# Kernel tuning notes

Measured on AMD Instinct MI355X. Metric: run time of the kernel, lower is better.

The kernel has to match this reference:

```python
import jax, jax.numpy as jnp
import numpy as np

B, T, D_MODEL, N_HEAD = 8, 1024, 1024, 8
D_K = D_MODEL // N_HEAD  # = d_v = 128; V projection shared across heads


def setup_inputs() -> dict:
    key = jax.random.key(0)
    ks = jax.random.split(key, 8)
    scale = 0.02
    q = jax.random.normal(ks[0], (B, T, D_MODEL), jnp.float32)
    k = jax.random.normal(ks[1], (B, T, D_MODEL), jnp.float32)
    v = jax.random.normal(ks[2], (B, T, D_MODEL), jnp.float32)
    # causal mask, 1.0 = attend, broadcast to batch (shape (B, T, T))
    mask = jnp.broadcast_to(jnp.tril(jnp.ones((T, T), jnp.float32)), (B, T, T))
    Wq = jax.random.normal(ks[3], (N_HEAD, D_MODEL, D_K), jnp.float32) * scale
    Wk = jax.random.normal(ks[4], (N_HEAD, D_MODEL, D_K), jnp.float32) * scale
    Wv = jax.random.normal(ks[5], (D_MODEL, D_K), jnp.float32) * scale  # shared across heads
    Wo = jax.random.normal(ks[6], (D_K, D_MODEL), jnp.float32) * scale
    return {"q": q, "k": k, "v": v, "mask": mask, "Wq": Wq, "Wk": Wk, "Wv": Wv, "Wo": Wo}


def reference(q, k, v, mask, Wq, Wk, Wv, Wo):
    # Per-head Q/K projections (batched over heads), shared V projection.
    qh = jnp.einsum('btd,hdk->hbtk', q, Wq)  # (H,B,T,d_k)
    kh = jnp.einsum('bsd,hdk->hbsk', k, Wk)  # (H,B,S,d_k)
    vh = jnp.einsum('bsd,dk->bsk', v, Wv)    # (B,S,d_v) shared across heads
    temper = jnp.sqrt(jnp.asarray(qh.shape[-1], jnp.float32))
    scores = jnp.einsum('hbtk,hbsk->hbts', qh, kh) / temper
    scores = scores + (-1e9) * (1.0 - mask)[None]  # additive mask per head
    attn = jax.nn.softmax(scores, axis=-1)          # (H,B,T,S)
    heads = jnp.einsum('hbts,bsk->hbtk', attn, vh)  # (H,B,T,d_v)
    out = jnp.einsum('btk,kd->btd', heads.mean(axis=0), Wo)  # mean over heads, then w_o
    return out, attn  # dropout rate 0.0 / inference -> identity
```

## Files before the change

### kernel.cpp

```cpp
#include <hip/hip_runtime.h>
#include <cstdint>

typedef __attribute__((ext_vector_type(8))) short bf16x8;
typedef __attribute__((ext_vector_type(4))) float f32x4;

constexpr int NH = 8, NB = 8, SEQ = 1024, DM = 1024, DK = 128;
constexpr int MTOT = NB * SEQ;

__device__ __forceinline__ unsigned short f2bf(float f) {
    unsigned int u = __float_as_uint(f);
    unsigned int r = (u + 0x7fffu + ((u >> 16) & 1u)) >> 16;
    return (unsigned short)r;
}
__device__ __forceinline__ float bf2f(unsigned int s) {
    return __uint_as_float((s & 0xffffu) << 16);
}
__device__ __forceinline__ void gld16(const void* g, void* l) {
    __builtin_amdgcn_global_load_lds((const __attribute__((address_space(1))) void*)g,
                                     (__attribute__((address_space(3))) void*)l, 16, 0, 0);
}

__global__ __launch_bounds__(256) void transpose_w_kernel(
    const float* __restrict__ Wq, const float* __restrict__ Wk,
    const float* __restrict__ Wv, const float* __restrict__ Wo,
    unsigned short* __restrict__ WqT, unsigned short* __restrict__ WkT,
    unsigned short* __restrict__ WvT, unsigned short* __restrict__ WoT)
{
    const int s = blockIdx.y;
    const float* in; unsigned short* out; int R, C;
    if (s < 8)        { in = Wq + (size_t)s * DM * DK;       out = WqT + (size_t)s * DK * DM;       R = DM; C = DK; }
    else if (s < 16)  { in = Wk + (size_t)(s - 8) * DM * DK; out = WkT + (size_t)(s - 8) * DK * DM; R = DM; C = DK; }
    else if (s == 16) { in = Wv; out = WvT; R = DM; C = DK; }
    else              { in = Wo; out = WoT; R = DK; C = DM; }
    const int tc = C / 32;
    const int r0 = (blockIdx.x / tc) * 32, c0 = (blockIdx.x % tc) * 32;
    __shared__ unsigned short t[32][33];
    const int tid = threadIdx.x;
    const int a = tid >> 3, b4 = (tid & 7) * 4;
    float4 f = *reinterpret_cast<const float4*>(&in[(size_t)(r0 + a) * C + c0 + b4]);
    t[a][b4 + 0] = f2bf(f.x); t[a][b4 + 1] = f2bf(f.y);
    t[a][b4 + 2] = f2bf(f.z); t[a][b4 + 3] = f2bf(f.w);
    __syncthreads();
    ushort4 o;
    o.x = t[b4 + 0][a]; o.y = t[b4 + 1][a]; o.z = t[b4 + 2][a]; o.w = t[b4 + 3][a];
    *reinterpret_cast<ushort4*>(&out[(size_t)(c0 + a) * R + r0 + b4]) = o;
}

__global__ __launch_bounds__(256) void cvt_kernel(
    const float* __restrict__ q, const float* __restrict__ k, const float* __restrict__ v,
    unsigned short* __restrict__ qb, unsigned short* __restrict__ kb,
    unsigned short* __restrict__ vb)
{
    const float* src; unsigned short* dst;
    const int s = blockIdx.y;
    if (s == 0)      { src = q; dst = qb; }
    else if (s == 1) { src = k; dst = kb; }
    else             { src = v; dst = vb; }
    const size_t base = ((size_t)blockIdx.x * 256 + threadIdx.x) * 8;
    float4 f0 = *reinterpret_cast<const float4*>(&src[base]);
    float4 f1 = *reinterpret_cast<const float4*>(&src[base + 4]);
    uint4 o;
    o.x = (unsigned int)f2bf(f0.x) | ((unsigned int)f2bf(f0.y) << 16);
    o.y = (unsigned int)f2bf(f0.z) | ((unsigned int)f2bf(f0.w) << 16);
    o.z = (unsigned int)f2bf(f1.x) | ((unsigned int)f2bf(f1.y) << 16);
    o.w = (unsigned int)f2bf(f1.z) | ((unsigned int)f2bf(f1.w) << 16);
    *reinterpret_cast<uint4*>(&dst[base]) = o;
}

__global__ __launch_bounds__(256) void proj_kernel(
    const unsigned short* __restrict__ qb, const unsigned short* __restrict__ kb,
    const unsigned short* __restrict__ vb,
    const unsigned short* __restrict__ WqT, const unsigned short* __restrict__ WkT,
    const unsigned short* __restrict__ WvT,
    unsigned short* __restrict__ qh, unsigned short* __restrict__ kh,
    unsigned short* __restrict__ vt)
{
    const int g = blockIdx.x, m0 = blockIdx.y * 128;
    const unsigned short* Ab; const unsigned short* Bt;
    if (g < 8)       { Ab = qb; Bt = WqT + (size_t)g * DK * DM; }
    else if (g < 16) { Ab = kb; Bt = WkT + (size_t)(g - 8) * DK * DM; }
    else             { Ab = vb; Bt = WvT; }

    __shared__ unsigned short As[128][32];
    __shared__ unsigned short Bs[128][32];

    const int tid = threadIdx.x, wave = tid >> 6, lane = tid & 63, quad = lane >> 4, l15 = lane & 15;
    const int wm = (wave & 1) * 64, wn = (wave >> 1) * 64;

    f32x4 acc[4][4];
    for (int mi = 0; mi < 4; ++mi)
        for (int ni = 0; ni < 4; ++ni)
            acc[mi][ni] = (f32x4){0.f, 0.f, 0.f, 0.f};

    const unsigned short* gA0 = Ab + (size_t)(m0 + (tid >> 2)) * DM + (tid & 3) * 8;
    const unsigned short* gB0 = Bt + (size_t)(tid >> 2) * DM + (tid & 3) * 8;
    char* lA = (char*)&As[0][0] + wave * 1024;
    char* lB = (char*)&Bs[0][0] + wave * 1024;

    for (int k0 = 0; k0 < DM; k0 += 32) {
        __syncthreads();
        gld16(gA0 + k0, lA); gld16(gA0 + k0 + 64 * DM, lA + 4096);
        gld16(gB0 + k0, lB); gld16(gB0 + k0 + 64 * DM, lB + 4096);
        __syncthreads();
        bf16x8 af[4], bfr[4];
        for (int mi = 0; mi < 4; ++mi)
            af[mi] = *reinterpret_cast<const bf16x8*>(&As[wm + mi * 16 + l15][quad * 8]);
        for (int ni = 0; ni < 4; ++ni)
            bfr[ni] = *reinterpret_cast<const bf16x8*>(&Bs[wn + ni * 16 + l15][quad * 8]);
        for (int mi = 0; mi < 4; ++mi)
            for (int ni = 0; ni < 4; ++ni)
                acc[mi][ni] = __builtin_amdgcn_mfma_f32_16x16x32_bf16(af[mi], bfr[ni], acc[mi][ni], 0, 0, 0);
    }

    if (g < 16) {
        unsigned short* C = (g < 8) ? (qh + (size_t)g * MTOT * DK)
                                    : (kh + (size_t)(g - 8) * MTOT * DK);
        for (int mi = 0; mi < 4; ++mi)
            for (int ni = 0; ni < 4; ++ni)
                for (int r = 0; r < 4; ++r)
                    C[(size_t)(m0 + wm + mi * 16 + quad * 4 + r) * DK + wn + ni * 16 + l15] =
                        f2bf(acc[mi][ni][r]);
    } else {
        for (int mi = 0; mi < 4; ++mi)
            for (int ni = 0; ni < 4; ++ni)
                for (int r = 0; r < 4; ++r) {
                    int row = m0 + wm + mi * 16 + quad * 4 + r;
                    int col = wn + ni * 16 + l15;
                    vt[((size_t)(row >> 10) * DK + col) * SEQ + (row & 1023)] = f2bf(acc[mi][ni][r]);
                }
    }
}

__global__ __launch_bounds__(256) void attn_kernel(
    const unsigned short* __restrict__ qh, const unsigned short* __restrict__ kh,
    const unsigned short* __restrict__ vt, unsigned short* __restrict__ heads,
    float* __restrict__ attn)
{
    const int p = blockIdx.x, hb = blockIdx.y, b = hb & 7;
    const unsigned short* kbase = kh + (size_t)hb * SEQ * DK;
    const unsigned short* vbase = vt + (size_t)b * DK * SEQ;

    __shared__ unsigned short Ks[4][64][32];
    __shared__ unsigned short Ps[64][72];

    const int tid = threadIdx.x, wave = tid >> 6, lane = tid & 63, quad = lane >> 4, l15 = lane & 15;
    const float scale = 0.08838834764831843f;

    const unsigned short* gK0 = kbase + (size_t)(tid >> 2) * DK + (tid & 3) * 8;
    char* lK = (char*)&Ks[0][0][0] + wave * 1024;

    for (int tt = 0; tt < 2; ++tt) {
        const int ti = tt ? (15 - p) : p;
        const unsigned short* qbase = qh + ((size_t)hb * SEQ + ti * 64) * DK;
        float* attn_base            = attn + ((size_t)hb * SEQ + ti * 64) * SEQ;
        unsigned short* hbase       = heads + ((size_t)hb * SEQ + ti * 64) * DK;

        bf16x8 aq[4];
        for (int ks = 0; ks < 4; ++ks)
            aq[ks] = *reinterpret_cast<const bf16x8*>(
                &qbase[(size_t)(wave * 16 + l15) * DK + ks * 32 + quad * 8]);

        const int trow_base = ti * 64 + wave * 16 + quad * 4;
        float l_run[4] = {0.f, 0.f, 0.f, 0.f};

        for (int j = 0; j <= ti; ++j) {
            __syncthreads();
            const unsigned short* gKj = gK0 + (size_t)j * 64 * DK;
            for (int ks = 0; ks < 4; ++ks) gld16(gKj + ks * 32, lK + ks * 4096);
            __syncthreads();
            f32x4 sacc[4];
            for (int ni = 0; ni < 4; ++ni) sacc[ni] = (f32x4){0.f, 0.f, 0.f, 0.f};
            for (int ks = 0; ks < 4; ++ks)
                for (int ni = 0; ni < 4; ++ni) {
                    bf16x8 bb = *reinterpret_cast<const bf16x8*>(&Ks[ks][ni * 16 + l15][quad * 8]);
                    sacc[ni] = __builtin_amdgcn_mfma_f32_16x16x32_bf16(aq[ks], bb, sacc[ni], 0, 0, 0);
                }
            const bool diag = (j == ti);
            for (int r = 0; r < 4; ++r) {
                float lsum = 0.f;
                for (int ni = 0; ni < 4; ++ni) {
                    int s = j * 64 + ni * 16 + l15;
                    float e = __expf(sacc[ni][r] * scale);
                    lsum += (!diag || s <= trow_base + r) ? e : 0.f;
                }
                for (int off = 1; off < 16; off <<= 1)
                    lsum += __shfl_xor(lsum, off, 64);
                l_run[r] += lsum;
            }
        }

        float inv_l[4];
        for (int r = 0; r < 4; ++r) inv_l[r] = 1.f / l_run[r];
        f32x4 oacc[8];
        for (int n = 0; n < 8; ++n) oacc[n] = (f32x4){0.f, 0.f, 0.f, 0.f};

        for (int j = 0; j <= ti; ++j) {
            __syncthreads();
            const unsigned short* gKj = gK0 + (size_t)j * 64 * DK;
            for (int ks = 0; ks < 4; ++ks) gld16(gKj + ks * 32, lK + ks * 4096);
            __syncthreads();
            f32x4 sacc[4];
            for (int ni = 0; ni < 4; ++ni) sacc[ni] = (f32x4){0.f, 0.f, 0.f, 0.f};
            for (int ks = 0; ks < 4; ++ks)
                for (int ni = 0; ni < 4; ++ni) {
                    bf16x8 bb = *reinterpret_cast<const bf16x8*>(&Ks[ks][ni * 16 + l15][quad * 8]);
                    sacc[ni] = __builtin_amdgcn_mfma_f32_16x16x32_bf16(aq[ks], bb, sacc[ni], 0, 0, 0);
                }
            const bool diag = (j == ti);
            for (int r = 0; r < 4; ++r)
                for (int ni = 0; ni < 4; ++ni) {
                    int s = j * 64 + ni * 16 + l15;
                    float pv = (!diag || s <= trow_base + r)
                                  ? __expf(sacc[ni][r] * scale) * inv_l[r] : 0.f;
                    Ps[wave * 16 + quad * 4 + r][ni * 16 + l15] = f2bf(pv);
                }
            __syncthreads();
            {
                int row = tid >> 2, c0 = (tid & 3) * 16;
                uint4 u0 = *reinterpret_cast<const uint4*>(&Ps[row][c0]);
                uint4 u1 = *reinterpret_cast<const uint4*>(&Ps[row][c0 + 8]);
                float* dst = attn_base + (size_t)row * SEQ + j * 64 + c0;
                f32x4 f0 = {bf2f(u0.x), bf2f(u0.x >> 16), bf2f(u0.y), bf2f(u0.y >> 16)};
                f32x4 f1 = {bf2f(u0.z), bf2f(u0.z >> 16), bf2f(u0.w), bf2f(u0.w >> 16)};
                f32x4 f2 = {bf2f(u1.x), bf2f(u1.x >> 16), bf2f(u1.y), bf2f(u1.y >> 16)};
                f32x4 f3 = {bf2f(u1.z), bf2f(u1.z >> 16), bf2f(u1.w), bf2f(u1.w >> 16)};
                __builtin_nontemporal_store(f0, (f32x4*)(dst));
                __builtin_nontemporal_store(f1, (f32x4*)(dst + 4));
                __builtin_nontemporal_store(f2, (f32x4*)(dst + 8));
                __builtin_nontemporal_store(f3, (f32x4*)(dst + 12));
            }
            for (int ks2 = 0; ks2 < 2; ++ks2) {
                bf16x8 ap = *reinterpret_cast<const bf16x8*>(&Ps[wave * 16 + l15][ks2 * 32 + quad * 8]);
                for (int n2 = 0; n2 < 8; ++n2) {
                    bf16x8 bv = *reinterpret_cast<const bf16x8*>(
                        &vbase[(size_t)(n2 * 16 + l15) * SEQ + j * 64 + ks2 * 32 + quad * 8]);
                    oacc[n2] = __builtin_amdgcn_mfma_f32_16x16x32_bf16(ap, bv, oacc[n2], 0, 0, 0);
                }
            }
        }

        for (int n2 = 0; n2 < 8; ++n2)
            for (int r = 0; r < 4; ++r)
                hbase[(size_t)(wave * 16 + quad * 4 + r) * DK + n2 * 16 + l15] = f2bf(oacc[n2][r]);

        {
            const int s0 = (ti + 1) * 64;
            if (s0 < SEQ) {
                const int z4 = (SEQ - s0) >> 2;
                f32x4 zz = {0.f, 0.f, 0.f, 0.f};
                for (int r = 0; r < 64; ++r)
                    for (int c = tid; c < z4; c += 256)
                        __builtin_nontemporal_store(zz, (f32x4*)&attn_base[(size_t)r * SEQ + s0 + c * 4]);
            }
        }
    }
}

__global__ __launch_bounds__(256) void mean_kernel(
    const unsigned short* __restrict__ heads, unsigned short* __restrict__ hmean)
{
    size_t base = ((size_t)blockIdx.x * 256 + threadIdx.x) * 8;
    float s[8] = {0.f, 0.f, 0.f, 0.f, 0.f, 0.f, 0.f, 0.f};
    for (int h = 0; h < 8; ++h) {
        uint4 u = *reinterpret_cast<const uint4*>(&heads[(size_t)h * MTOT * DK + base]);
        s[0] += bf2f(u.x); s[1] += bf2f(u.x >> 16);
        s[2] += bf2f(u.y); s[3] += bf2f(u.y >> 16);
        s[4] += bf2f(u.z); s[5] += bf2f(u.z >> 16);
        s[6] += bf2f(u.w); s[7] += bf2f(u.w >> 16);
    }
    uint4 o;
    o.x = (unsigned int)f2bf(s[0] * 0.125f) | ((unsigned int)f2bf(s[1] * 0.125f) << 16);
    o.y = (unsigned int)f2bf(s[2] * 0.125f) | ((unsigned int)f2bf(s[3] * 0.125f) << 16);
    o.z = (unsigned int)f2bf(s[4] * 0.125f) | ((unsigned int)f2bf(s[5] * 0.125f) << 16);
    o.w = (unsigned int)f2bf(s[6] * 0.125f) | ((unsigned int)f2bf(s[7] * 0.125f) << 16);
    *reinterpret_cast<uint4*>(&hmean[base]) = o;
}

__global__ __launch_bounds__(256) void out_kernel(
    const unsigned short* __restrict__ hmean, const unsigned short* __restrict__ WoT,
    float* __restrict__ out)
{
    const int n0 = blockIdx.x * 128, m0 = blockIdx.y * 128;
    __shared__ unsigned short As[128][32];
    __shared__ unsigned short Bs[128][32];

    const int tid = threadIdx.x, wave = tid >> 6, lane = tid & 63, quad = lane >> 4, l15 = lane & 15;
    const int wm = (wave & 1) * 64, wn = (wave >> 1) * 64;

    f32x4 acc[4][4];
    for (int mi = 0; mi < 4; ++mi)
        for (int ni = 0; ni < 4; ++ni)
            acc[mi][ni] = (f32x4){0.f, 0.f, 0.f, 0.f};

    const unsigned short* gA0 = hmean + (size_t)(m0 + (tid >> 2)) * DK + (tid & 3) * 8;
    const unsigned short* gB0 = WoT + (size_t)(n0 + (tid >> 2)) * DK + (tid & 3) * 8;
    char* lA = (char*)&As[0][0] + wave * 1024;
    char* lB = (char*)&Bs[0][0] + wave * 1024;

    for (int k0 = 0; k0 < DK; k0 += 32) {
        __syncthreads();
        gld16(gA0 + k0, lA); gld16(gA0 + k0 + 64 * DK, lA + 4096);
        gld16(gB0 + k0, lB); gld16(gB0 + k0 + 64 * DK, lB + 4096);
        __syncthreads();
        bf16x8 af[4], bfr[4];
        for (int mi = 0; mi < 4; ++mi)
            af[mi] = *reinterpret_cast<const bf16x8*>(&As[wm + mi * 16 + l15][quad * 8]);
        for (int ni = 0; ni < 4; ++ni)
            bfr[ni] = *reinterpret_cast<const bf16x8*>(&Bs[wn + ni * 16 + l15][quad * 8]);
        for (int mi = 0; mi < 4; ++mi)
            for (int ni = 0; ni < 4; ++ni)
                acc[mi][ni] = __builtin_amdgcn_mfma_f32_16x16x32_bf16(af[mi], bfr[ni], acc[mi][ni], 0, 0, 0);
    }
    for (int mi = 0; mi < 4; ++mi)
        for (int ni = 0; ni < 4; ++ni)
            for (int r = 0; r < 4; ++r)
                out[(size_t)(m0 + wm + mi * 16 + quad * 4 + r) * DM + n0 + wn + ni * 16 + l15] =
                    acc[mi][ni][r];
}

extern "C" void kernel_launch(void* const* d_in, const int* in_sizes, int n_in,
                              void* d_out, int out_size, void* d_ws, size_t ws_size,
                              hipStream_t stream) {
    (void)in_sizes; (void)n_in; (void)out_size; (void)ws_size;
    const float* q  = (const float*)d_in[0];
    const float* k  = (const float*)d_in[1];
    const float* v  = (const float*)d_in[2];
    const float* Wq = (const float*)d_in[4];
    const float* Wk = (const float*)d_in[5];
    const float* Wv = (const float*)d_in[6];
    const float* Wo = (const float*)d_in[7];

    float* out  = (float*)d_out;
    float* attn = out + (size_t)NB * SEQ * DM;
    unsigned short* heads = (unsigned short*)d_out;
    unsigned short* qb = (unsigned short*)attn;
    unsigned short* kb = qb + (size_t)MTOT * DM;
    unsigned short* vb = kb + (size_t)MTOT * DM;

    unsigned short* ws    = (unsigned short*)d_ws;
    unsigned short* WqT   = ws;
    unsigned short* WkT   = WqT + (size_t)NH * DK * DM;
    unsigned short* WvT   = WkT + (size_t)NH * DK * DM;
    unsigned short* WoT   = WvT + (size_t)DK * DM;
    unsigned short* qh    = WoT + (size_t)DM * DK;
    unsigned short* kh    = qh + (size_t)NH * MTOT * DK;
    unsigned short* vt    = kh + (size_t)NH * MTOT * DK;
    unsigned short* hmean = vt + (size_t)NB * DK * SEQ;

    transpose_w_kernel<<<dim3(128, 18), 256, 0, stream>>>(Wq, Wk, Wv, Wo, WqT, WkT, WvT, WoT);
    cvt_kernel<<<dim3(4096, 3), 256, 0, stream>>>(q, k, v, qb, kb, vb);
    proj_kernel<<<dim3(17, 64), 256, 0, stream>>>(qb, kb, vb, WqT, WkT, WvT, qh, kh, vt);
    attn_kernel<<<dim3(8, 64), 256, 0, stream>>>(qh, kh, vt, heads, attn);
    mean_kernel<<<512, 256, 0, stream>>>(heads, hmean);
    out_kernel<<<dim3(8, 64), 256, 0, stream>>>(hmean, WoT, out);
}
```

Baseline: 615.8 us.

## Double-buffer LDS loads, swizzle layout, and run both attention tiles concurrently per block

The projection GEMM now double-buffers its A/B tiles in LDS and applies an XOR swizzle to cut bank conflicts, with one barrier per k-step. The attention kernel switches to 512-thread blocks in which two 256-thread groups handle the paired causal tiles (p and 15-p) at the same time, sharing double-buffered K tiles. It also writes attention probabilities to global directly from registers instead of staging them through LDS. The aim is to overlap global loads with MFMA work and raise occupancy, at the cost of more LDS, idle lanes in the short-tile group, and scalar rather than vectorised attn stores.

```diff
diff --git a/kernel.cpp b/kernel.cpp
--- a/kernel.cpp
+++ b/kernel.cpp
@@ -81,8 +81,8 @@
     else if (g < 16) { Ab = kb; Bt = WkT + (size_t)(g - 8) * DK * DM; }
     else             { Ab = vb; Bt = WvT; }
 
-    __shared__ unsigned short As[128][32];
-    __shared__ unsigned short Bs[128][32];
+    __shared__ unsigned short As[2][128][32];
+    __shared__ unsigned short Bs[2][128][32];
 
     const int tid = threadIdx.x, wave = tid >> 6, lane = tid & 63, quad = lane >> 4, l15 = lane & 15;
     const int wm = (wave & 1) * 64, wn = (wave >> 1) * 64;
@@ -92,24 +92,38 @@
         for (int ni = 0; ni < 4; ++ni)
             acc[mi][ni] = (f32x4){0.f, 0.f, 0.f, 0.f};
 
-    const unsigned short* gA0 = Ab + (size_t)(m0 + (tid >> 2)) * DM + (tid & 3) * 8;
-    const unsigned short* gB0 = Bt + (size_t)(tid >> 2) * DM + (tid & 3) * 8;
-    char* lA = (char*)&As[0][0] + wave * 1024;
-    char* lB = (char*)&Bs[0][0] + wave * 1024;
-
+    const int s_row = tid >> 2;
+    const int s_col = ((tid & 3) ^ ((s_row >> 1) & 3)) * 8;
+    const unsigned short* gA = Ab + (size_t)(m0 + s_row) * DM + s_col;
+    const unsigned short* gAh = Ab + (size_t)(m0 + 64 + s_row) * DM + s_col;
+    const unsigned short* gB = Bt + (size_t)s_row * DM + s_col;
+    const unsigned short* gBh = Bt + (size_t)(64 + s_row) * DM + s_col;
+    char* lA = (char*)&As[0][0][0] + wave * 1024;
+    char* lB = (char*)&Bs[0][0][0] + wave * 1024;
+    const int rcb = (quad ^ ((l15 >> 1) & 3)) * 8;
+
+    auto STAGE = [&](int k0, int bsel) {
+        gld16(gA + k0, lA + bsel * 8192);
+        gld16(gAh + k0, lA + bsel * 8192 + 4096);
+        gld16(gB + k0, lB + bsel * 8192);
+        gld16(gBh + k0, lB + bsel * 8192 + 4096);
+    };
+
+    int bsel = 0;
+    STAGE(0, 0);
+    __syncthreads();
     for (int k0 = 0; k0 < DM; k0 += 32) {
-        __syncthreads();
-        gld16(gA0 + k0, lA); gld16(gA0 + k0 + 64 * DM, lA + 4096);
-        gld16(gB0 + k0, lB); gld16(gB0 + k0 + 64 * DM, lB + 4096);
-        __syncthreads();
+        if (k0 + 32 < DM) STAGE(k0 + 32, bsel ^ 1);
         bf16x8 af[4], bfr[4];
         for (int mi = 0; mi < 4; ++mi)
-            af[mi] = *reinterpret_cast<const bf16x8*>(&As[wm + mi * 16 + l15][quad * 8]);
-        for (int ni = 0; ni < 4; ++ni)
-            bfr[ni] = *reinterpret_cast<const bf16x8*>(&Bs[wn + ni * 16 + l15][quad * 8]);
+            af[mi] = *reinterpret_cast<const bf16x8*>(&As[bsel][wm + mi * 16 + l15][rcb]);
+        for (int ni = 0; ni < 4; ++ni)
+            bfr[ni] = *reinterpret_cast<const bf16x8*>(&Bs[bsel][wn + ni * 16 + l15][rcb]);
         for (int mi = 0; mi < 4; ++mi)
             for (int ni = 0; ni < 4; ++ni)
                 acc[mi][ni] = __builtin_amdgcn_mfma_f32_16x16x32_bf16(af[mi], bfr[ni], acc[mi][ni], 0, 0, 0);
+        __syncthreads();
+        bsel ^= 1;
     }
 
     if (g < 16) {
@@ -131,48 +145,73 @@
     }
 }
 
-__global__ __launch_bounds__(256) void attn_kernel(
+__global__ __launch_bounds__(512, 4) void attn_kernel(
     const unsigned short* __restrict__ qh, const unsigned short* __restrict__ kh,
     const unsigned short* __restrict__ vt, unsigned short* __restrict__ heads,
     float* __restrict__ attn)
 {
-    const int p = blockIdx.x, hb = blockIdx.y, b = hb & 7;
+    const int id = blockIdx.y * 8 + blockIdx.x;
+    const int hi = (id >> 8) & 1;
+    const int p  = ((id & 7) + hi * 4) & 7;
+    const int hb = hi * 32 + ((id >> 3) & 31);
+    const int b  = hb & 7;
+
+    const int tid = threadIdx.x;
+    const int wg = tid >> 8;
+    const int lt = tid & 255;
+    const int w8 = tid >> 6;
+    const int lw = w8 & 3;
+    const int lane = tid & 63, quad = lane >> 4, l15 = lane & 15;
+
+    const int ti = wg ? (15 - p) : p;
+    const int JMAX = 15 - p;
+
     const unsigned short* kbase = kh + (size_t)hb * SEQ * DK;
     const unsigned short* vbase = vt + (size_t)b * DK * SEQ;
-
-    __shared__ unsigned short Ks[4][64][32];
-    __shared__ unsigned short Ps[64][72];
-
-    const int tid = threadIdx.x, wave = tid >> 6, lane = tid & 63, quad = lane >> 4, l15 = lane & 15;
+    const unsigned short* qbase = qh + ((size_t)hb * SEQ + ti * 64) * DK;
+    float* attn_base            = attn + ((size_t)hb * SEQ + ti * 64) * SEQ;
+    unsigned short* hbase       = heads + ((size_t)hb * SEQ + ti * 64) * DK;
+
+    __shared__ unsigned short Ks[2][4][64][32];
+    __shared__ unsigned short Ps[2][64][72];
+
     const float scale = 0.08838834764831843f;
 
-    const unsigned short* gK0 = kbase + (size_t)(tid >> 2) * DK + (tid & 3) * 8;
-    char* lK = (char*)&Ks[0][0][0] + wave * 1024;
-
-    for (int tt = 0; tt < 2; ++tt) {
-        const int ti = tt ? (15 - p) : p;
-        const unsigned short* qbase = qh + ((size_t)hb * SEQ + ti * 64) * DK;
-        float* attn_base            = attn + ((size_t)hb * SEQ + ti * 64) * SEQ;
-        unsigned short* hbase       = heads + ((size_t)hb * SEQ + ti * 64) * DK;
-
-        bf16x8 aq[4];
-        for (int ks = 0; ks < 4; ++ks)
-            aq[ks] = *reinterpret_cast<const bf16x8*>(
-                &qbase[(size_t)(wave * 16 + l15) * DK + ks * 32 + quad * 8]);
-
-        const int trow_base = ti * 64 + wave * 16 + quad * 4;
-        float l_run[4] = {0.f, 0.f, 0.f, 0.f};
-
-        for (int j = 0; j <= ti; ++j) {
-            __syncthreads();
-            const unsigned short* gKj = gK0 + (size_t)j * 64 * DK;
-            for (int ks = 0; ks < 4; ++ks) gld16(gKj + ks * 32, lK + ks * 4096);
-            __syncthreads();
+    const int s_rg  = w8 & 3;
+    const int s_ks0 = w8 >> 2;
+    const int s_row = s_rg * 16 + (lane >> 2);
+    const int s_col = ((lane & 3) ^ ((s_row >> 1) & 3)) * 8;
+    const unsigned short* gK = kbase + (size_t)s_row * DK + s_col;
+    char* d0base = (char*)&Ks[0][s_ks0][s_rg * 16][0];
+    char* d1base = (char*)&Ks[0][s_ks0 + 2][s_rg * 16][0];
+
+    auto STAGE = [&](int j, int bsel) {
+        const unsigned short* src = gK + (size_t)j * 64 * DK;
+        gld16(src + s_ks0 * 32, d0base + bsel * 16384);
+        gld16(src + (s_ks0 + 2) * 32, d1base + bsel * 16384);
+    };
+
+    const int rcb = (quad ^ ((l15 >> 1) & 3)) * 8;
+
+    bf16x8 aq[4];
+    for (int ks = 0; ks < 4; ++ks)
+        aq[ks] = *reinterpret_cast<const bf16x8*>(
+            &qbase[(size_t)(lw * 16 + l15) * DK + ks * 32 + quad * 8]);
+
+    const int trow_base = ti * 64 + lw * 16 + quad * 4;
+    float l_run[4] = {0.f, 0.f, 0.f, 0.f};
+
+    int bsel = 0;
+    STAGE(0, 0);
+    __syncthreads();
+    for (int j = 0; j <= JMAX; ++j) {
+        if (j < JMAX) STAGE(j + 1, bsel ^ 1);
+        if (j <= ti) {
             f32x4 sacc[4];
             for (int ni = 0; ni < 4; ++ni) sacc[ni] = (f32x4){0.f, 0.f, 0.f, 0.f};
             for (int ks = 0; ks < 4; ++ks)
                 for (int ni = 0; ni < 4; ++ni) {
-                    bf16x8 bb = *reinterpret_cast<const bf16x8*>(&Ks[ks][ni * 16 + l15][quad * 8]);
+                    bf16x8 bb = *reinterpret_cast<const bf16x8*>(&Ks[bsel][ks][ni * 16 + l15][rcb]);
                     sacc[ni] = __builtin_amdgcn_mfma_f32_16x16x32_bf16(aq[ks], bb, sacc[ni], 0, 0, 0);
                 }
             const bool diag = (j == ti);
@@ -188,22 +227,25 @@
                 l_run[r] += lsum;
             }
         }
-
-        float inv_l[4];
-        for (int r = 0; r < 4; ++r) inv_l[r] = 1.f / l_run[r];
-        f32x4 oacc[8];
-        for (int n = 0; n < 8; ++n) oacc[n] = (f32x4){0.f, 0.f, 0.f, 0.f};
-
-        for (int j = 0; j <= ti; ++j) {
-            __syncthreads();
-            const unsigned short* gKj = gK0 + (size_t)j * 64 * DK;
-            for (int ks = 0; ks < 4; ++ks) gld16(gKj + ks * 32, lK + ks * 4096);
-            __syncthreads();
+        __syncthreads();
+        bsel ^= 1;
+    }
+
+    float inv_l[4];
+    for (int r = 0; r < 4; ++r) inv_l[r] = 1.f / l_run[r];
+    f32x4 oacc[8];
+    for (int n = 0; n < 8; ++n) oacc[n] = (f32x4){0.f, 0.f, 0.f, 0.f};
+
+    STAGE(0, bsel);
+    __syncthreads();
+    for (int j = 0; j <= JMAX; ++j) {
+        if (j < JMAX) STAGE(j + 1, bsel ^ 1);
+        if (j <= ti) {
             f32x4 sacc[4];
             for (int ni = 0; ni < 4; ++ni) sacc[ni] = (f32x4){0.f, 0.f, 0.f, 0.f};
             for (int ks = 0; ks < 4; ++ks)
                 for (int ni = 0; ni < 4; ++ni) {
-                    bf16x8 bb = *reinterpret_cast<const bf16x8*>(&Ks[ks][ni * 16 + l15][quad * 8]);
+                    bf16x8 bb = *reinterpret_cast<const bf16x8*>(&Ks[bsel][ks][ni * 16 + l15][rcb]);
                     sacc[ni] = __builtin_amdgcn_mfma_f32_16x16x32_bf16(aq[ks], bb, sacc[ni], 0, 0, 0);
                 }
             const bool diag = (j == ti);
@@ -212,25 +254,12 @@
                     int s = j * 64 + ni * 16 + l15;
                     float pv = (!diag || s <= trow_base + r)
                                   ? __expf(sacc[ni][r] * scale) * inv_l[r] : 0.f;
-                    Ps[wave * 16 + quad * 4 + r][ni * 16 + l15] = f2bf(pv);
-                }
-            __syncthreads();
-            {
-                int row = tid >> 2, c0 = (tid & 3) * 16;
-                uint4 u0 = *reinterpret_cast<const uint4*>(&Ps[row][c0]);
-                uint4 u1 = *reinterpret_cast<const uint4*>(&Ps[row][c0 + 8]);
-                float* dst = attn_base + (size_t)row * SEQ + j * 64 + c0;
-                f32x4 f0 = {bf2f(u0.x), bf2f(u0.x >> 16), bf2f(u0.y), bf2f(u0.y >> 16)};
-                f32x4 f1 = {bf2f(u0.z), bf2f(u0.z >> 16), bf2f(u0.w), bf2f(u0.w >> 16)};
-                f32x4 f2 = {bf2f(u1.x), bf2f(u1.x >> 16), bf2f(u1.y), bf2f(u1.y >> 16)};
-                f32x4 f3 = {bf2f(u1.z), bf2f(u1.z >> 16), bf2f(u1.w), bf2f(u1.w >> 16)};
-                __builtin_nontemporal_store(f0, (f32x4*)(dst));
-                __builtin_nontemporal_store(f1, (f32x4*)(dst + 4));
-                __builtin_nontemporal_store(f2, (f32x4*)(dst + 8));
-                __builtin_nontemporal_store(f3, (f32x4*)(dst + 12));
-            }
+                    __builtin_nontemporal_store(
+                        pv, &attn_base[(size_t)(lw * 16 + quad * 4 + r) * SEQ + s]);
+                    Ps[wg][lw * 16 + quad * 4 + r][ni * 16 + l15] = f2bf(pv);
+                }
             for (int ks2 = 0; ks2 < 2; ++ks2) {
-                bf16x8 ap = *reinterpret_cast<const bf16x8*>(&Ps[wave * 16 + l15][ks2 * 32 + quad * 8]);
+                bf16x8 ap = *reinterpret_cast<const bf16x8*>(&Ps[wg][lw * 16 + l15][ks2 * 32 + quad * 8]);
                 for (int n2 = 0; n2 < 8; ++n2) {
                     bf16x8 bv = *reinterpret_cast<const bf16x8*>(
                         &vbase[(size_t)(n2 * 16 + l15) * SEQ + j * 64 + ks2 * 32 + quad * 8]);
@@ -238,20 +267,22 @@
                 }
             }
         }
-
-        for (int n2 = 0; n2 < 8; ++n2)
-            for (int r = 0; r < 4; ++r)
-                hbase[(size_t)(wave * 16 + quad * 4 + r) * DK + n2 * 16 + l15] = f2bf(oacc[n2][r]);
-
-        {
-            const int s0 = (ti + 1) * 64;
-            if (s0 < SEQ) {
-                const int z4 = (SEQ - s0) >> 2;
-                f32x4 zz = {0.f, 0.f, 0.f, 0.f};
-                for (int r = 0; r < 64; ++r)
-                    for (int c = tid; c < z4; c += 256)
-                        __builtin_nontemporal_store(zz, (f32x4*)&attn_base[(size_t)r * SEQ + s0 + c * 4]);
-            }
+        __syncthreads();
+        bsel ^= 1;
+    }
+
+    for (int n2 = 0; n2 < 8; ++n2)
+        for (int r = 0; r < 4; ++r)
+            hbase[(size_t)(lw * 16 + quad * 4 + r) * DK + n2 * 16 + l15] = f2bf(oacc[n2][r]);
+
+    {
+        const int s0 = (ti + 1) * 64;
+        if (s0 < SEQ) {
+            const int z4 = (SEQ - s0) >> 2;
+            f32x4 zz = {0.f, 0.f, 0.f, 0.f};
+            for (int r = 0; r < 64; ++r)
+                for (int c = lt; c < z4; c += 256)
+                    __builtin_nontemporal_store(zz, (f32x4*)&attn_base[(size_t)r * SEQ + s0 + c * 4]);
         }
     }
 }
@@ -350,7 +381,7 @@
     transpose_w_kernel<<<dim3(128, 18), 256, 0, stream>>>(Wq, Wk, Wv, Wo, WqT, WkT, WvT, WoT);
     cvt_kernel<<<dim3(4096, 3), 256, 0, stream>>>(q, k, v, qb, kb, vb);
     proj_kernel<<<dim3(17, 64), 256, 0, stream>>>(qb, kb, vb, WqT, WkT, WvT, qh, kh, vt);
-    attn_kernel<<<dim3(8, 64), 256, 0, stream>>>(qh, kh, vt, heads, attn);
+    attn_kernel<<<dim3(8, 64), 512, 0, stream>>>(qh, kh, vt, heads, attn);
     mean_kernel<<<512, 256, 0, stream>>>(heads, hmean);
     out_kernel<<<dim3(8, 64), 256, 0, stream>>>(hmean, WoT, out);
 }
```

Measured after the change: 615.1 us. About the same (-0.1%).
